# Kernel optimization log

Hardware: AMD Instinct MI355X
Metric: run time of the kernel (lower is better)

Reference implementation:

```python
import jax, jax.numpy as jnp
import numpy as np

N = 20_000_000
B = 16_384


def setup_inputs() -> dict:
    key = jax.random.key(0)
    k1, k2, k3 = jax.random.split(key, 3)
    inp = jax.random.normal(k1, (N,), dtype=jnp.float32)
    tgt = jax.random.normal(k2, (N,), dtype=jnp.float32)
    batch = jnp.sort(jax.random.randint(k3, (N,), 0, B, dtype=jnp.int64))
    return {"input": inp, "target": tgt, "batch": batch, "batch_size": B}


def reference(input, target, batch, batch_size):
    # sum_j c_ij @ c_ij.T over a segment == (segment_sum c)^2
    seg_in = jax.ops.segment_sum(input, batch, num_segments=batch_size)
    seg_tg = jax.ops.segment_sum(target, batch, num_segments=batch_size)
    dot_in = seg_in * seg_in          # [B]
    dot_tg = seg_tg * seg_tg          # [B]
    loss_dot = jnp.sum((dot_in - dot_tg) ** 2)            # F.mse_loss(..., 'sum')
    loss_elem = jnp.sum((jnp.abs(input) - jnp.abs(target)) ** 2)
    return loss_dot + loss_elem
```

## Files before the change

kernel.cpp:

```cpp
#include <hip/hip_runtime.h>

#define BSEG   16384
#define NPART  256
#define CHUNK  4
#define WS_BYTES (2 * BSEG * 4 + NPART * 8)

__global__ __launch_bounds__(256) void main_pass(
        const float* __restrict__ in, const float* __restrict__ tg,
        const int* __restrict__ batch,
        float* __restrict__ seg_in, float* __restrict__ seg_tg,
        double* __restrict__ elem_part, int n)
{
    const int tid  = blockIdx.x * blockDim.x + threadIdx.x;
    const int lane = threadIdx.x & 63;
    const long long i0 = (long long)tid * CHUNK;
    const bool live = (i0 < n);

    float4 a, t; int4 c;
    if (live) {
        a = *reinterpret_cast<const float4*>(in + i0);
        t = *reinterpret_cast<const float4*>(tg + i0);
        c = *reinterpret_cast<const int4*>(batch + i0);
    }

    float elem = 0.0f;
    int   cur  = -1;
    float si = 0.0f, st = 0.0f;

    if (live) {
        float vi[CHUNK] = {a.x, a.y, a.z, a.w};
        float vt[CHUNK] = {t.x, t.y, t.z, t.w};
        int   vb[CHUNK] = {c.x, c.y, c.z, c.w};
        cur = vb[0];
        #pragma unroll
        for (int j = 0; j < CHUNK; ++j) {
            float x = vi[j], y = vt[j];
            float d = fabsf(x) - fabsf(y);
            elem = fmaf(d, d, elem);
            int b = vb[j];
            if (b != cur) {
                atomicAdd(seg_in + cur, si);
                atomicAdd(seg_tg + cur, st);
                cur = b; si = 0.0f; st = 0.0f;
            }
            si += x; st += y;
        }
    }

    #pragma unroll
    for (int d = 1; d < 64; d <<= 1) {
        float o1 = __shfl_up(si, d);
        float o2 = __shfl_up(st, d);
        int  oid = __shfl_up(cur, d);
        if (lane >= d && oid == cur) { si += o1; st += o2; }
    }
    const int  nextId = __shfl_down(cur, 1);
    const bool isTail = (lane == 63) || (nextId != cur);
    if (isTail && cur >= 0) {
        atomicAdd(seg_in + cur, si);
        atomicAdd(seg_tg + cur, st);
    }

    #pragma unroll
    for (int off = 32; off; off >>= 1) elem += __shfl_xor(elem, off);
    __shared__ float wsum[4];
    int wid = threadIdx.x >> 6;
    if (lane == 0) wsum[wid] = elem;
    __syncthreads();
    if (threadIdx.x == 0) {
        float s = wsum[0] + wsum[1] + wsum[2] + wsum[3];
        atomicAdd(elem_part + (blockIdx.x & (NPART - 1)), (double)s);
    }
}

__global__ __launch_bounds__(1024) void finalize_kernel(
        const float* __restrict__ seg_in, const float* __restrict__ seg_tg,
        const double* __restrict__ elem_part, float* __restrict__ out)
{
    const float4* s4 = (const float4*)seg_in;
    const float4* g4 = (const float4*)seg_tg;
    double acc = 0.0;
    for (int i = threadIdx.x; i < BSEG / 4; i += 1024) {
        float4 a = s4[i], b = g4[i];
        float d0 = a.x * a.x - b.x * b.x;
        float d1 = a.y * a.y - b.y * b.y;
        float d2 = a.z * a.z - b.z * b.z;
        float d3 = a.w * a.w - b.w * b.w;
        acc += (double)d0 * d0 + (double)d1 * d1 + (double)d2 * d2 + (double)d3 * d3;
    }
    if (threadIdx.x < NPART) acc += elem_part[threadIdx.x];
    #pragma unroll
    for (int off = 32; off; off >>= 1) acc += __shfl_xor(acc, off);
    __shared__ double wsum[16];
    int lane = threadIdx.x & 63, wid = threadIdx.x >> 6;
    if (lane == 0) wsum[wid] = acc;
    __syncthreads();
    if (threadIdx.x == 0) {
        double t = 0.0;
        #pragma unroll
        for (int w = 0; w < 16; ++w) t += wsum[w];
        out[0] = (float)t;
    }
}

extern "C" void kernel_launch(void* const* d_in, const int* in_sizes, int n_in,
                              void* d_out, int out_size, void* d_ws, size_t ws_size,
                              hipStream_t stream) {
    const float* in    = (const float*)d_in[0];
    const float* tg    = (const float*)d_in[1];
    const int*   batch = (const int*)d_in[2];
    const int n = in_sizes[0];

    float*  seg_in    = (float*)d_ws;
    float*  seg_tg    = seg_in + BSEG;
    double* elem_part = (double*)(seg_in + 2 * BSEG);
    float*  out       = (float*)d_out;

    hipMemsetAsync(d_ws, 0, WS_BYTES, stream);

    const int nthreads = n / CHUNK;
    const int blocks   = (nthreads + 255) / 256;
    main_pass<<<blocks, 256, 0, stream>>>(in, tg, batch, seg_in, seg_tg, elem_part, n);

    finalize_kernel<<<1, 1024, 0, stream>>>(seg_in, seg_tg, elem_part, out);
}
```

Measured before the change: 232.1 us.

## Replace atomic segment scatter with binary-searched per-segment wave reduction

A small kernel binary-searches the sorted batch array to find where each segment starts. The main kernel then gives each segment one wavefront. That wavefront reduces its input and target sums and the elementwise term, and squares the segment-sum difference locally. This stops the full batch array from being streamed and removes the per-segment float atomics and the dense segment arrays the finalize step used to read. In exchange it relies on batch being sorted, and per-wave work depends on segment size, which can cause imbalance for skewed segments.

Result: no change. 231.4 us (-0.3%).

```diff
diff --git a/kernel.cpp b/kernel.cpp
--- a/kernel.cpp
+++ b/kernel.cpp
@@ -2,105 +2,95 @@
 
 #define BSEG   16384
 #define NPART  256
-#define CHUNK  4
-#define WS_BYTES (2 * BSEG * 4 + NPART * 8)
 
-__global__ __launch_bounds__(256) void main_pass(
+__global__ __launch_bounds__(256) void seg_bounds(
+        const int* __restrict__ batch, int n, int* __restrict__ seg_start)
+{
+    int s = blockIdx.x * 256 + threadIdx.x;
+    if (s > BSEG) return;
+    if (s == BSEG) { seg_start[s] = n; return; }
+    int lo = 0, hi = n;
+    while (lo < hi) {
+        int mid = (lo + hi) >> 1;
+        if (batch[mid] < s) lo = mid + 1; else hi = mid;
+    }
+    seg_start[s] = lo;
+}
+
+__global__ __launch_bounds__(256) void seg_sum(
         const float* __restrict__ in, const float* __restrict__ tg,
-        const int* __restrict__ batch,
-        float* __restrict__ seg_in, float* __restrict__ seg_tg,
-        double* __restrict__ elem_part, int n)
+        const int* __restrict__ seg_start, double* __restrict__ elem_part)
 {
-    const int tid  = blockIdx.x * blockDim.x + threadIdx.x;
     const int lane = threadIdx.x & 63;
-    const long long i0 = (long long)tid * CHUNK;
-    const bool live = (i0 < n);
+    const int wid  = threadIdx.x >> 6;
+    const int s    = blockIdx.x * 4 + wid;
 
-    float4 a, t; int4 c;
-    if (live) {
-        a = *reinterpret_cast<const float4*>(in + i0);
-        t = *reinterpret_cast<const float4*>(tg + i0);
-        c = *reinterpret_cast<const int4*>(batch + i0);
+    const int lo = seg_start[s], hi = seg_start[s + 1];
+
+    float si = 0.f, st = 0.f, elem = 0.f;
+
+    const int head = min(hi, (lo + 3) & ~3);
+    int i = lo + lane;
+    if (i < head) {
+        float x = in[i], y = tg[i];
+        si += x; st += y;
+        float d = fabsf(x) - fabsf(y);
+        elem = fmaf(d, d, elem);
     }
-
-    float elem = 0.0f;
-    int   cur  = -1;
-    float si = 0.0f, st = 0.0f;
-
-    if (live) {
-        float vi[CHUNK] = {a.x, a.y, a.z, a.w};
-        float vt[CHUNK] = {t.x, t.y, t.z, t.w};
-        int   vb[CHUNK] = {c.x, c.y, c.z, c.w};
-        cur = vb[0];
-        #pragma unroll
-        for (int j = 0; j < CHUNK; ++j) {
-            float x = vi[j], y = vt[j];
-            float d = fabsf(x) - fabsf(y);
-            elem = fmaf(d, d, elem);
-            int b = vb[j];
-            if (b != cur) {
-                atomicAdd(seg_in + cur, si);
-                atomicAdd(seg_tg + cur, st);
-                cur = b; si = 0.0f; st = 0.0f;
-            }
-            si += x; st += y;
-        }
+    const int nb = (hi - head) >> 2;
+    for (int k = lane; k < nb; k += 64) {
+        const int base = head + (k << 2);
+        float4 a = *reinterpret_cast<const float4*>(in + base);
+        float4 b = *reinterpret_cast<const float4*>(tg + base);
+        si += a.x + a.y + a.z + a.w;
+        st += b.x + b.y + b.z + b.w;
+        float d0 = fabsf(a.x) - fabsf(b.x);
+        float d1 = fabsf(a.y) - fabsf(b.y);
+        float d2 = fabsf(a.z) - fabsf(b.z);
+        float d3 = fabsf(a.w) - fabsf(b.w);
+        elem = fmaf(d0, d0, elem); elem = fmaf(d1, d1, elem);
+        elem = fmaf(d2, d2, elem); elem = fmaf(d3, d3, elem);
+    }
+    const int tail = head + (nb << 2);
+    i = tail + lane;
+    if (i < hi) {
+        float x = in[i], y = tg[i];
+        si += x; st += y;
+        float d = fabsf(x) - fabsf(y);
+        elem = fmaf(d, d, elem);
     }
 
     #pragma unroll
-    for (int d = 1; d < 64; d <<= 1) {
-        float o1 = __shfl_up(si, d);
-        float o2 = __shfl_up(st, d);
-        int  oid = __shfl_up(cur, d);
-        if (lane >= d && oid == cur) { si += o1; st += o2; }
-    }
-    const int  nextId = __shfl_down(cur, 1);
-    const bool isTail = (lane == 63) || (nextId != cur);
-    if (isTail && cur >= 0) {
-        atomicAdd(seg_in + cur, si);
-        atomicAdd(seg_tg + cur, st);
+    for (int off = 32; off; off >>= 1) {
+        si   += __shfl_xor(si, off);
+        st   += __shfl_xor(st, off);
+        elem += __shfl_xor(elem, off);
     }
 
-    #pragma unroll
-    for (int off = 32; off; off >>= 1) elem += __shfl_xor(elem, off);
-    __shared__ float wsum[4];
-    int wid = threadIdx.x >> 6;
-    if (lane == 0) wsum[wid] = elem;
+    __shared__ double wacc[4];
+    if (lane == 0) {
+        float d = si * si - st * st;
+        wacc[wid] = (double)d * (double)d + (double)elem;
+    }
     __syncthreads();
     if (threadIdx.x == 0) {
-        float s = wsum[0] + wsum[1] + wsum[2] + wsum[3];
-        atomicAdd(elem_part + (blockIdx.x & (NPART - 1)), (double)s);
+        atomicAdd(elem_part + (blockIdx.x & (NPART - 1)),
+                  wacc[0] + wacc[1] + wacc[2] + wacc[3]);
     }
 }
 
-__global__ __launch_bounds__(1024) void finalize_kernel(
-        const float* __restrict__ seg_in, const float* __restrict__ seg_tg,
+__global__ __launch_bounds__(256) void finalize_kernel(
         const double* __restrict__ elem_part, float* __restrict__ out)
 {
-    const float4* s4 = (const float4*)seg_in;
-    const float4* g4 = (const float4*)seg_tg;
-    double acc = 0.0;
-    for (int i = threadIdx.x; i < BSEG / 4; i += 1024) {
-        float4 a = s4[i], b = g4[i];
-        float d0 = a.x * a.x - b.x * b.x;
-        float d1 = a.y * a.y - b.y * b.y;
-        float d2 = a.z * a.z - b.z * b.z;
-        float d3 = a.w * a.w - b.w * b.w;
-        acc += (double)d0 * d0 + (double)d1 * d1 + (double)d2 * d2 + (double)d3 * d3;
-    }
-    if (threadIdx.x < NPART) acc += elem_part[threadIdx.x];
+    double v = elem_part[threadIdx.x];
     #pragma unroll
-    for (int off = 32; off; off >>= 1) acc += __shfl_xor(acc, off);
-    __shared__ double wsum[16];
+    for (int off = 32; off; off >>= 1) v += __shfl_xor(v, off);
+    __shared__ double wsum[4];
     int lane = threadIdx.x & 63, wid = threadIdx.x >> 6;
-    if (lane == 0) wsum[wid] = acc;
+    if (lane == 0) wsum[wid] = v;
     __syncthreads();
-    if (threadIdx.x == 0) {
-        double t = 0.0;
-        #pragma unroll
-        for (int w = 0; w < 16; ++w) t += wsum[w];
-        out[0] = (float)t;
-    }
+    if (threadIdx.x == 0)
+        out[0] = (float)(wsum[0] + wsum[1] + wsum[2] + wsum[3]);
 }
 
 extern "C" void kernel_launch(void* const* d_in, const int* in_sizes, int n_in,
@@ -111,16 +101,13 @@
     const int*   batch = (const int*)d_in[2];
     const int n = in_sizes[0];
 
-    float*  seg_in    = (float*)d_ws;
-    float*  seg_tg    = seg_in + BSEG;
-    double* elem_part = (double*)(seg_in + 2 * BSEG);
+    double* elem_part = (double*)d_ws;
+    int*    seg_start = (int*)((char*)d_ws + NPART * 8);
     float*  out       = (float*)d_out;
 
-    hipMemsetAsync(d_ws, 0, WS_BYTES, stream);
+    hipMemsetAsync(d_ws, 0, NPART * 8, stream);
 
-    const int nthreads = n / CHUNK;
-    const int blocks   = (nthreads + 255) / 256;
-    main_pass<<<blocks, 256, 0, stream>>>(in, tg, batch, seg_in, seg_tg, elem_part, n);
-
-    finalize_kernel<<<1, 1024, 0, stream>>>(seg_in, seg_tg, elem_part, out);
+    seg_bounds<<<(BSEG + 1 + 255) / 256, 256, 0, stream>>>(batch, n, seg_start);
+    seg_sum<<<BSEG / 4, 256, 0, stream>>>(in, tg, seg_start, elem_part);
+    finalize_kernel<<<1, 256, 0, stream>>>(elem_part, out);
 }
```
